# Optimization experiments

Measured on AMD Instinct MI355X. Metric: run time of the kernel, lower is better.

The kernel has to match this reference:

```python
import jax, jax.numpy as jnp
import numpy as np

B, D, V = 64, 2048, 128000


def setup_inputs() -> dict:
    key = jax.random.key(0)
    k_hs, k_w, k_t, k_g, k_m = jax.random.split(key, 5)
    hidden_states = jax.random.normal(k_hs, (B, D), dtype=jnp.float32)
    weight = jax.random.normal(k_w, (V, D), dtype=jnp.float32) * 0.02
    # temperatures in [0.5, 1.5) to avoid divide-by-~0
    temperature = jax.random.uniform(k_t, (B,), dtype=jnp.float32, minval=0.5, maxval=1.5)
    # gumbel-max noise for categorical sampling of non-greedy rows
    u = jax.random.uniform(k_g, (B, V), dtype=jnp.float32, minval=1e-10, maxval=1.0)
    gumbel = -jnp.log(-jnp.log(u))
    lm_head_indices = jnp.arange(B, dtype=jnp.int64)
    greedy_mask = jax.random.randint(k_m, (B,), 0, 2).astype(jnp.bool_)
    return {
        "hidden_states": hidden_states,
        "weight": weight,
        "temperature": temperature,
        "gumbel": gumbel,
        "lm_head_indices": lm_head_indices,
        "greedy_mask": greedy_mask,
    }


def reference(hidden_states, weight, temperature, gumbel, lm_head_indices, greedy_mask):
    # gather the rows whose next token we must sample
    hs = hidden_states[lm_head_indices]                      # [B, D]
    logits = jnp.einsum("bd,vd->bv", hs, weight).astype(jnp.float32)  # [B, V]
    logits = logits / temperature[:, None]                   # temperature scaling
    logp = jax.nn.log_softmax(logits, axis=-1)               # [B, V]
    probs = jnp.exp(logp)
    # greedy rows: top_k = 1 -> argmax; non-greedy: top_k = 1<<30, top_p = 1.0
    # -> sample from full distribution (gumbel-max trick)
    greedy_ids = jnp.argmax(probs, axis=-1)
    sampled_ids = jnp.argmax(logp + gumbel, axis=-1)
    next_token_ids = jnp.where(greedy_mask, greedy_ids, sampled_ids).astype(jnp.int64)
    # gather chosen prob and take log (log_softmax gather == log(prob gather))
    chosen_logprobs = jnp.take_along_axis(logp, next_token_ids[:, None], axis=-1)[:, 0]
    return next_token_ids, chosen_logprobs
```

## Files before the change

kernel.cpp:

```cpp
#include <hip/hip_runtime.h>
#include <stdint.h>

#define B_ROWS 64
#define D_DIM  2048
#define V_DIM  128000
#define N_TILE 128
#define NBLK   (V_DIM / N_TILE)
#define KCH    (D_DIM / 32)

typedef float  f32x4  __attribute__((ext_vector_type(4)));
typedef __bf16 bf16x8 __attribute__((ext_vector_type(8)));

__global__ void prep_A(const float* __restrict__ hs, const int* __restrict__ idx,
                       __bf16* __restrict__ Ah, __bf16* __restrict__ Al)
{
    const int b   = blockIdx.x;
    const int tid = threadIdx.x;
    const int row = idx[b];
    const int k0  = tid * 8;
    const float* src = hs + (long)row * D_DIM + k0;
    const int c    = tid >> 2;
    const int quad = tid & 3;
    const int t    = b >> 4;
    const int lane = quad * 16 + (b & 15);
    const long off = ((long)(c * 4 + t) * 64 + lane) * 8;
    bf16x8 vh, vl;
#pragma unroll
    for (int j = 0; j < 8; j++) {
        float x = src[j];
        __bf16 h = (__bf16)x;
        vh[j] = h;
        vl[j] = (__bf16)(x - (float)h);
    }
    *(bf16x8*)(Ah + off) = vh;
    *(bf16x8*)(Al + off) = vl;
}

__global__ void gemm_sample(const float* __restrict__ W,
                            const __bf16* __restrict__ Ah,
                            const __bf16* __restrict__ Al,
                            const float* __restrict__ temp,
                            const float* __restrict__ gum,
                            f32x4* __restrict__ partA,
                            float* __restrict__ partB)
{
    __shared__ float smem[8256];
    const int tid  = threadIdx.x;
    const int wid  = tid >> 6;
    const int lane = tid & 63;
    const int v0   = blockIdx.x * N_TILE;

    float* wreg = smem + wid * 2048;

    const int srow = lane >> 3;
    const int spb  = lane & 7;

    auto stage = [&](int c, int buf) {
        float* lb = wreg + buf * 1024;
#pragma unroll
        for (int cc = 0; cc < 4; cc++) {
            int rl   = cc * 8 + srow;
            int kblk = spb ^ (rl & 7);
            const float* g = W + (long)(v0 + wid * 32 + rl) * D_DIM + c * 32 + kblk * 4;
            __builtin_amdgcn_global_load_lds(
                (const __attribute__((address_space(1))) void*)g,
                (__attribute__((address_space(3))) void*)(lb + cc * 256),
                16, 0, 0);
        }
    };

    f32x4 acc[4][2];
#pragma unroll
    for (int t = 0; t < 4; t++)
#pragma unroll
        for (int u = 0; u < 2; u++)
            acc[t][u] = (f32x4){0.f, 0.f, 0.f, 0.f};

    const int r0 = lane & 15;
    const int q  = lane >> 4;
    const __bf16* aph = Ah + lane * 8;
    const __bf16* apl = Al + lane * 8;

    stage(0, 0);
    for (int c = 0; c < KCH; c++) {
        const int buf = c & 1;
        if (c + 1 < KCH) {
            stage(c + 1, buf ^ 1);
            asm volatile("s_waitcnt vmcnt(4)" ::: "memory");
        } else {
            asm volatile("s_waitcnt vmcnt(0)" ::: "memory");
        }
        bf16x8 ah[4], al[4];
#pragma unroll
        for (int t = 0; t < 4; t++) {
            ah[t] = *(const bf16x8*)(aph + (long)(c * 4 + t) * 512);
            al[t] = *(const bf16x8*)(apl + (long)(c * 4 + t) * 512);
        }
        const float* lb = wreg + buf * 1024;
#pragma unroll
        for (int u = 0; u < 2; u++) {
            const int r = u * 16 + r0;
            const float* rp = lb + r * 32;
            f32x4 w0 = *(const f32x4*)(rp + (((2 * q)     ^ (r & 7)) * 4));
            f32x4 w1 = *(const f32x4*)(rp + (((2 * q + 1) ^ (r & 7)) * 4));
            bf16x8 wh, wl;
#pragma unroll
            for (int j = 0; j < 4; j++) {
                float x = w0[j];
                __bf16 h = (__bf16)x;
                wh[j] = h; wl[j] = (__bf16)(x - (float)h);
            }
#pragma unroll
            for (int j = 0; j < 4; j++) {
                float x = w1[j];
                __bf16 h = (__bf16)x;
                wh[4 + j] = h; wl[4 + j] = (__bf16)(x - (float)h);
            }
#pragma unroll
            for (int t = 0; t < 4; t++) {
                acc[t][u] = __builtin_amdgcn_mfma_f32_16x16x32_bf16(ah[t], wh, acc[t][u], 0, 0, 0);
                acc[t][u] = __builtin_amdgcn_mfma_f32_16x16x32_bf16(al[t], wh, acc[t][u], 0, 0, 0);
                acc[t][u] = __builtin_amdgcn_mfma_f32_16x16x32_bf16(ah[t], wl, acc[t][u], 0, 0, 0);
            }
        }
    }

    __syncthreads();
#pragma unroll
    for (int t = 0; t < 4; t++)
#pragma unroll
        for (int u = 0; u < 2; u++)
#pragma unroll
            for (int r = 0; r < 4; r++) {
                int m = t * 16 + q * 4 + r;
                int n = wid * 32 + u * 16 + r0;
                smem[m * 129 + n] = acc[t][u][r];
            }
    __syncthreads();

    const int brow = tid >> 2;
    const int qq   = tid & 3;
    const float invT = 1.0f / temp[brow];
    const float* lrow = smem + brow * 129;
    const float* grow = gum + (long)brow * V_DIM + v0;

    float gmax = -INFINITY; int gidx = 0;
    float smax = -INFINITY; int sidx = 0;
#pragma unroll 8
    for (int i = 0; i < 32; i++) {
        int col = qq + 4 * i;
        float L = lrow[col];
        if (L > gmax) { gmax = L; gidx = col; }
        float s = L * invT + grow[col];
        if (s > smax) { smax = s; sidx = col; }
    }
#pragma unroll
    for (int d = 1; d < 4; d <<= 1) {
        float og = __shfl_xor(gmax, d); int oi = __shfl_xor(gidx, d);
        if (og > gmax || (og == gmax && oi < gidx)) { gmax = og; gidx = oi; }
        float os = __shfl_xor(smax, d); int si = __shfl_xor(sidx, d);
        if (os > smax || (os == smax && si < sidx)) { smax = os; sidx = si; }
    }
    float lsum = 0.f;
#pragma unroll 8
    for (int i = 0; i < 32; i++) {
        int col = qq + 4 * i;
        lsum += __expf((lrow[col] - gmax) * invT);
    }
    lsum += __shfl_xor(lsum, 1);
    lsum += __shfl_xor(lsum, 2);
    if (qq == 0) {
        f32x4 p;
        p[0] = gmax; p[1] = __int_as_float(v0 + gidx);
        p[2] = smax; p[3] = __int_as_float(v0 + sidx);
        partA[(long)brow * NBLK + blockIdx.x] = p;
        partB[(long)brow * NBLK + blockIdx.x] = lsum;
    }
}

__global__ void finalize(const f32x4* __restrict__ partA, const float* __restrict__ partB,
                         const float* __restrict__ temp, const int* __restrict__ gmask,
                         const float* __restrict__ gum, float* __restrict__ out)
{
    const int b = blockIdx.x;
    const int tid = threadIdx.x;
    const float invT = 1.0f / temp[b];
    float mg = -INFINITY; int ig = 0;
    float ms = -INFINITY; int is_ = 0;
    float mx = -INFINITY; float sm = 0.f;
    for (int i = tid; i < NBLK; i += 256) {
        f32x4 p = partA[(long)b * NBLK + i];
        float ls = partB[(long)b * NBLK + i];
        int vi = __float_as_int(p[1]);
        if (p[0] > mg || (p[0] == mg && vi < ig)) { mg = p[0]; ig = vi; }
        int si = __float_as_int(p[3]);
        if (p[2] > ms || (p[2] == ms && si < is_)) { ms = p[2]; is_ = si; }
        float m2 = p[0] * invT;
        if (m2 > mx) { sm = sm * __expf(mx - m2) + ls; mx = m2; }
        else         { sm = sm + ls * __expf(m2 - mx); }
    }
#pragma unroll
    for (int d = 1; d < 64; d <<= 1) {
        float og = __shfl_xor(mg, d); int oi = __shfl_xor(ig, d);
        if (og > mg || (og == mg && oi < ig)) { mg = og; ig = oi; }
        float os = __shfl_xor(ms, d); int si = __shfl_xor(is_, d);
        if (os > ms || (os == ms && si < is_)) { ms = os; is_ = si; }
        float omx = __shfl_xor(mx, d); float osm = __shfl_xor(sm, d);
        if (omx > mx) { sm = sm * __expf(mx - omx) + osm; mx = omx; }
        else          { sm = sm + osm * __expf(omx - mx); }
    }
    __shared__ float red[4][8];
    const int w = tid >> 6;
    if ((tid & 63) == 0) {
        red[w][0] = mg; red[w][1] = __int_as_float(ig);
        red[w][2] = ms; red[w][3] = __int_as_float(is_);
        red[w][4] = mx; red[w][5] = sm;
    }
    __syncthreads();
    if (tid == 0) {
#pragma unroll
        for (int w2 = 1; w2 < 4; w2++) {
            float og = red[w2][0]; int oi = __float_as_int(red[w2][1]);
            if (og > mg || (og == mg && oi < ig)) { mg = og; ig = oi; }
            float os = red[w2][2]; int si = __float_as_int(red[w2][3]);
            if (os > ms || (os == ms && si < is_)) { ms = os; is_ = si; }
            float omx = red[w2][4], osm = red[w2][5];
            if (omx > mx) { sm = sm * __expf(mx - omx) + osm; mx = omx; }
            else          { sm = sm + osm * __expf(omx - mx); }
        }
        float logZ = mx + logf(sm);
        int id; float lp;
        if (gmask[b] != 0) { id = ig; lp = mg * invT - logZ; }
        else { id = is_; lp = (ms - gum[(long)b * V_DIM + is_]) - logZ; }
        out[b] = (float)id;
        out[B_ROWS + b] = lp;
    }
}

extern "C" void kernel_launch(void* const* d_in, const int* in_sizes, int n_in,
                              void* d_out, int out_size, void* d_ws, size_t ws_size,
                              hipStream_t stream)
{
    (void)in_sizes; (void)n_in; (void)out_size; (void)ws_size;
    const float* hs   = (const float*)d_in[0];
    const float* W    = (const float*)d_in[1];
    const float* temp = (const float*)d_in[2];
    const float* gum  = (const float*)d_in[3];
    const int*   idx  = (const int*)d_in[4];
    const int*   mask = (const int*)d_in[5];
    float* out = (float*)d_out;

    char* ws = (char*)d_ws;
    __bf16* Ah   = (__bf16*)ws;
    __bf16* Al   = (__bf16*)(ws + 262144);
    f32x4*  pA   = (f32x4*)(ws + 524288);
    float*  pB   = (float*)(ws + 524288 + 1024000);

    prep_A     <<<B_ROWS, 256, 0, stream>>>(hs, idx, Ah, Al);
    gemm_sample<<<NBLK,   256, 0, stream>>>(W, Ah, Al, temp, gum, pA, pB);
    finalize   <<<B_ROWS, 256, 0, stream>>>(pA, pB, temp, mask, gum, out);
}
```

Before: 1.404 ms.

## Load weight tiles directly into registers with double-buffered prefetch instead of LDS

Drops the async global-to-LDS staging of the fp32 weight tile. Each lane now reads its own weight fragments straight from global memory into registers, with a two-deep software prefetch of both the A and W fragments. The aim is to cut LDS traffic, s_waitcnt stalls and LDS bank pressure, and to overlap global loads with MFMA work. In exchange it raises register pressure, and each lane does 32-byte strided row reads that may coalesce less well than the staged path. It also removes the __syncthreads before the epilogue smem write and adds __launch_bounds__(256).

```diff
diff --git a/kernel.cpp b/kernel.cpp
--- a/kernel.cpp
+++ b/kernel.cpp
@@ -36,13 +36,14 @@
     *(bf16x8*)(Al + off) = vl;
 }
 
-__global__ void gemm_sample(const float* __restrict__ W,
-                            const __bf16* __restrict__ Ah,
-                            const __bf16* __restrict__ Al,
-                            const float* __restrict__ temp,
-                            const float* __restrict__ gum,
-                            f32x4* __restrict__ partA,
-                            float* __restrict__ partB)
+__global__ void __launch_bounds__(256)
+gemm_sample(const float* __restrict__ W,
+            const __bf16* __restrict__ Ah,
+            const __bf16* __restrict__ Al,
+            const float* __restrict__ temp,
+            const float* __restrict__ gum,
+            f32x4* __restrict__ partA,
+            float* __restrict__ partB)
 {
     __shared__ float smem[8256];
     const int tid  = threadIdx.x;
@@ -50,24 +51,13 @@
     const int lane = tid & 63;
     const int v0   = blockIdx.x * N_TILE;
 
-    float* wreg = smem + wid * 2048;
-
-    const int srow = lane >> 3;
-    const int spb  = lane & 7;
-
-    auto stage = [&](int c, int buf) {
-        float* lb = wreg + buf * 1024;
-#pragma unroll
-        for (int cc = 0; cc < 4; cc++) {
-            int rl   = cc * 8 + srow;
-            int kblk = spb ^ (rl & 7);
-            const float* g = W + (long)(v0 + wid * 32 + rl) * D_DIM + c * 32 + kblk * 4;
-            __builtin_amdgcn_global_load_lds(
-                (const __attribute__((address_space(1))) void*)g,
-                (__attribute__((address_space(3))) void*)(lb + cc * 256),
-                16, 0, 0);
-        }
-    };
+    const int r0 = lane & 15;
+    const int q  = lane >> 4;
+
+    const float*  pw0 = W + (long)(v0 + wid * 32 + r0) * D_DIM + q * 8;
+    const float*  pw1 = pw0 + 16L * D_DIM;
+    const __bf16* pah = Ah + lane * 8;
+    const __bf16* pal = Al + lane * 8;
 
     f32x4 acc[4][2];
 #pragma unroll
@@ -76,56 +66,78 @@
         for (int u = 0; u < 2; u++)
             acc[t][u] = (f32x4){0.f, 0.f, 0.f, 0.f};
 
-    const int r0 = lane & 15;
-    const int q  = lane >> 4;
-    const __bf16* aph = Ah + lane * 8;
-    const __bf16* apl = Al + lane * 8;
-
-    stage(0, 0);
-    for (int c = 0; c < KCH; c++) {
-        const int buf = c & 1;
-        if (c + 1 < KCH) {
-            stage(c + 1, buf ^ 1);
-            asm volatile("s_waitcnt vmcnt(4)" ::: "memory");
-        } else {
-            asm volatile("s_waitcnt vmcnt(0)" ::: "memory");
-        }
-        bf16x8 ah[4], al[4];
+    bf16x8 ahA[4], alA[4], ahB[4], alB[4];
+    f32x4 wA0a, wA0b, wA1a, wA1b;
+    f32x4 wB0a, wB0b, wB1a, wB1b;
+
+    auto load_chunk = [&](bf16x8 (&ah)[4], bf16x8 (&al)[4],
+                          f32x4& w0a, f32x4& w0b, f32x4& w1a, f32x4& w1b) {
 #pragma unroll
         for (int t = 0; t < 4; t++) {
-            ah[t] = *(const bf16x8*)(aph + (long)(c * 4 + t) * 512);
-            al[t] = *(const bf16x8*)(apl + (long)(c * 4 + t) * 512);
-        }
-        const float* lb = wreg + buf * 1024;
-#pragma unroll
-        for (int u = 0; u < 2; u++) {
-            const int r = u * 16 + r0;
-            const float* rp = lb + r * 32;
-            f32x4 w0 = *(const f32x4*)(rp + (((2 * q)     ^ (r & 7)) * 4));
-            f32x4 w1 = *(const f32x4*)(rp + (((2 * q + 1) ^ (r & 7)) * 4));
+            ah[t] = *(const bf16x8*)(pah + t * 512);
+            al[t] = *(const bf16x8*)(pal + t * 512);
+        }
+        w0a = *(const f32x4*)(pw0);
+        w0b = *(const f32x4*)(pw0 + 4);
+        w1a = *(const f32x4*)(pw1);
+        w1b = *(const f32x4*)(pw1 + 4);
+        pah += 2048; pal += 2048;
+        pw0 += 32;   pw1 += 32;
+    };
+
+    auto compute = [&](bf16x8 (&ah)[4], bf16x8 (&al)[4],
+                       f32x4& w0a, f32x4& w0b, f32x4& w1a, f32x4& w1b) {
+        {
             bf16x8 wh, wl;
 #pragma unroll
             for (int j = 0; j < 4; j++) {
-                float x = w0[j];
-                __bf16 h = (__bf16)x;
+                float x = w0a[j]; __bf16 h = (__bf16)x;
                 wh[j] = h; wl[j] = (__bf16)(x - (float)h);
             }
 #pragma unroll
             for (int j = 0; j < 4; j++) {
-                float x = w1[j];
-                __bf16 h = (__bf16)x;
+                float x = w0b[j]; __bf16 h = (__bf16)x;
                 wh[4 + j] = h; wl[4 + j] = (__bf16)(x - (float)h);
             }
 #pragma unroll
             for (int t = 0; t < 4; t++) {
-                acc[t][u] = __builtin_amdgcn_mfma_f32_16x16x32_bf16(ah[t], wh, acc[t][u], 0, 0, 0);
-                acc[t][u] = __builtin_amdgcn_mfma_f32_16x16x32_bf16(al[t], wh, acc[t][u], 0, 0, 0);
-                acc[t][u] = __builtin_amdgcn_mfma_f32_16x16x32_bf16(ah[t], wl, acc[t][u], 0, 0, 0);
-            }
-        }
-    }
-
-    __syncthreads();
+                acc[t][0] = __builtin_amdgcn_mfma_f32_16x16x32_bf16(ah[t], wh, acc[t][0], 0, 0, 0);
+                acc[t][0] = __builtin_amdgcn_mfma_f32_16x16x32_bf16(al[t], wh, acc[t][0], 0, 0, 0);
+                acc[t][0] = __builtin_amdgcn_mfma_f32_16x16x32_bf16(ah[t], wl, acc[t][0], 0, 0, 0);
+            }
+        }
+        {
+            bf16x8 wh, wl;
+#pragma unroll
+            for (int j = 0; j < 4; j++) {
+                float x = w1a[j]; __bf16 h = (__bf16)x;
+                wh[j] = h; wl[j] = (__bf16)(x - (float)h);
+            }
+#pragma unroll
+            for (int j = 0; j < 4; j++) {
+                float x = w1b[j]; __bf16 h = (__bf16)x;
+                wh[4 + j] = h; wl[4 + j] = (__bf16)(x - (float)h);
+            }
+#pragma unroll
+            for (int t = 0; t < 4; t++) {
+                acc[t][1] = __builtin_amdgcn_mfma_f32_16x16x32_bf16(ah[t], wh, acc[t][1], 0, 0, 0);
+                acc[t][1] = __builtin_amdgcn_mfma_f32_16x16x32_bf16(al[t], wh, acc[t][1], 0, 0, 0);
+                acc[t][1] = __builtin_amdgcn_mfma_f32_16x16x32_bf16(ah[t], wl, acc[t][1], 0, 0, 0);
+            }
+        }
+    };
+
+    load_chunk(ahA, alA, wA0a, wA0b, wA1a, wA1b);
+    for (int c = 0; c < KCH - 2; c += 2) {
+        load_chunk(ahB, alB, wB0a, wB0b, wB1a, wB1b);
+        compute   (ahA, alA, wA0a, wA0b, wA1a, wA1b);
+        load_chunk(ahA, alA, wA0a, wA0b, wA1a, wA1b);
+        compute   (ahB, alB, wB0a, wB0b, wB1a, wB1b);
+    }
+    load_chunk(ahB, alB, wB0a, wB0b, wB1a, wB1b);
+    compute   (ahA, alA, wA0a, wA0b, wA1a, wA1b);
+    compute   (ahB, alB, wB0a, wB0b, wB1a, wB1b);
+
 #pragma unroll
     for (int t = 0; t < 4; t++)
 #pragma unroll
```

New measurement: 1.430 ms. No clear change (+1.9%).
